# Performance work log

Measured on AMD Instinct MI355X. Metric: run time of the kernel, lower is better.

The kernel has to match this reference:

```python
import jax, jax.numpy as jnp
import numpy as np

N_HEAD = 16
HEAD_DIM = 64
ROPE_BASE = 10000.0


def _rope(t):
    # t: [B, H, C, D]; rotate-half RoPE, offset 0
    B, H, C, D = t.shape
    inv_freq = 1.0 / (ROPE_BASE ** (jnp.arange(0, D, 2, dtype=jnp.float32) / D))  # [D/2]
    ang = jnp.arange(C, dtype=jnp.float32)[:, None] * inv_freq[None, :]           # [C, D/2]
    cos = jnp.concatenate([jnp.cos(ang), jnp.cos(ang)], axis=-1)                  # [C, D]
    sin = jnp.concatenate([jnp.sin(ang), jnp.sin(ang)], axis=-1)                  # [C, D]
    t1, t2 = jnp.split(t, 2, axis=-1)
    rot = jnp.concatenate([-t2, t1], axis=-1)
    return t * cos.astype(t.dtype) + rot * sin.astype(t.dtype)


def setup_inputs() -> dict:
    key = jax.random.key(0)
    ks = jax.random.split(key, 5)
    E = 1024
    B, C = 2, 2048
    s = 1.0 / np.sqrt(E)
    return {
        "x": jax.random.normal(ks[0], (B, C, E), dtype=jnp.float32),
        "Wq": jax.random.normal(ks[1], (E, E), dtype=jnp.float32) * s,
        "Wk": jax.random.normal(ks[2], (E, E), dtype=jnp.float32) * s,
        "Wv": jax.random.normal(ks[3], (E, E), dtype=jnp.float32) * s,
        "Wo": jax.random.normal(ks[4], (E, E), dtype=jnp.float32) * s,
    }


def reference(x, Wq, Wk, Wv, Wo):
    B, C, E = x.shape
    H, D = N_HEAD, HEAD_DIM
    # nn.Linear(bias=False): y = x @ W.T
    Q = (x @ Wq.T).reshape(B, C, H, D).transpose(0, 2, 1, 3)  # [B,H,C,D]
    K = (x @ Wk.T).reshape(B, C, H, D).transpose(0, 2, 1, 3)
    V = (x @ Wv.T).reshape(B, C, H, D).transpose(0, 2, 1, 3)
    Q = _rope(Q)
    K = _rope(K)
    scores = jnp.einsum("bhqd,bhkd->bhqk", Q, K) / jnp.sqrt(jnp.float32(D))
    causal = jnp.tril(jnp.ones((C, C), dtype=bool))
    scores = jnp.where(causal, scores, jnp.float32(-jnp.inf))
    weights = jax.nn.softmax(scores, axis=-1)
    hidden = jnp.einsum("bhqk,bhkd->bhqd", weights, V)
    hidden = hidden.transpose(0, 2, 1, 3).reshape(B, C, H * D)
    return hidden @ Wo.T
```

## Files before the change

kernel.cpp:

```cpp
#include <hip/hip_runtime.h>
#include <hip/hip_bf16.h>

typedef __attribute__((ext_vector_type(8))) short bf16x8;
typedef __attribute__((ext_vector_type(4))) float f32x4;
typedef unsigned short u16;
typedef unsigned int u32;


__device__ __forceinline__ u16 f2bf(float f) {
  __hip_bfloat16 h = __float2bfloat16(f);
  return *reinterpret_cast<u16*>(&h);
}

__device__ __forceinline__ void async16(const void* g, void* l) {
  __builtin_amdgcn_global_load_lds((const __attribute__((address_space(1))) u32*)g,
                                   (__attribute__((address_space(3))) u32*)l, 16, 0, 0);
}


__global__ void cast_bf16(const float4* __restrict__ src, ushort4* __restrict__ dst, int n4) {
  int stride = gridDim.x * blockDim.x;
  for (int i = blockIdx.x * blockDim.x + threadIdx.x; i < n4; i += stride) {
    float4 v = src[i];
    ushort4 o;
    o.x = f2bf(v.x); o.y = f2bf(v.y); o.z = f2bf(v.z); o.w = f2bf(v.w);
    dst[i] = o;
  }
}

__global__ void cast_w4(const float4* __restrict__ w0, const float4* __restrict__ w1,
                        const float4* __restrict__ w2, const float4* __restrict__ w3,
                        ushort4* __restrict__ o0, ushort4* __restrict__ o1,
                        ushort4* __restrict__ o2, ushort4* __restrict__ o3, int n4) {
  const float4* src = (blockIdx.y == 0) ? w0 : (blockIdx.y == 1) ? w1 : (blockIdx.y == 2) ? w2 : w3;
  ushort4* dst = (blockIdx.y == 0) ? o0 : (blockIdx.y == 1) ? o1 : (blockIdx.y == 2) ? o2 : o3;
  int stride = gridDim.x * blockDim.x;
  for (int i = blockIdx.x * blockDim.x + threadIdx.x; i < n4; i += stride) {
    float4 v = src[i];
    ushort4 o;
    o.x = f2bf(v.x); o.y = f2bf(v.y); o.z = f2bf(v.z); o.w = f2bf(v.w);
    dst[i] = o;
  }
}


__global__ void rope_table(float* __restrict__ tcos, float* __restrict__ tsin) {
  int idx = blockIdx.x * blockDim.x + threadIdx.x;
  if (idx >= 2048 * 32) return;
  int c = idx >> 5, j = idx & 31;
  float inv = powf(10000.f, -(float)j * (1.f / 32.f));
  float ang = (float)c * inv;
  tcos[idx] = cosf(ang);
  tsin[idx] = sinf(ang);
}


__launch_bounds__(256)
__global__ void qkv_gemm(const u16* __restrict__ xb, const u16* __restrict__ Wqb,
                         const u16* __restrict__ Wkb, const u16* __restrict__ Wvb,
                         const float* __restrict__ tcos, const float* __restrict__ tsin,
                         u16* __restrict__ Qr, u16* __restrict__ Kr, u16* __restrict__ Vt) {
  const int z = blockIdx.z;
  const u16* W = (z == 0) ? Wqb : (z == 1) ? Wkb : Wvb;
  u16* dst = (z == 0) ? Qr : (z == 1) ? Kr : Vt;
  const int m0 = blockIdx.y * 128, n0 = blockIdx.x * 128;
  const int tid = threadIdx.x, w = tid >> 6, lane = tid & 63, g = lane >> 4, cl = lane & 15;
  const int wr = w >> 1, wc = w & 1;
  __shared__ u16 As[128][32], Bs[128][32];
  f32x4 acc[4][4] = {};
  for (int k0 = 0; k0 < 1024; k0 += 32) {
#pragma unroll
    for (int ch = 0; ch < 2; ++ch) {
      int t = tid + ch * 256;
      int row = t >> 2, col = (t & 3) * 8;
      async16(&xb[(size_t)(m0 + row) * 1024 + k0 + col], &As[row][col]);
      async16(&W[(size_t)(n0 + row) * 1024 + k0 + col], &Bs[row][col]);
    }
    __syncthreads();
    bf16x8 af[4], bfr[4];
#pragma unroll
    for (int i = 0; i < 4; ++i) af[i] = *(const bf16x8*)&As[wr * 64 + i * 16 + cl][g * 8];
#pragma unroll
    for (int j = 0; j < 4; ++j) bfr[j] = *(const bf16x8*)&Bs[wc * 64 + j * 16 + cl][g * 8];
#pragma unroll
    for (int i = 0; i < 4; ++i)
#pragma unroll
      for (int j = 0; j < 4; ++j)
        acc[i][j] = __builtin_amdgcn_mfma_f32_16x16x32_bf16(af[i], bfr[j], acc[i][j], 0, 0, 0);
    __syncthreads();
  }
  if (z < 2) {
#pragma unroll
    for (int i = 0; i < 4; ++i) {
      int mbase = m0 + wr * 64 + i * 16 + g * 4;
#pragma unroll
      for (int r = 0; r < 4; ++r) {
        int mm = mbase + r;
        int b = mm >> 11, pos = mm & 2047;
#pragma unroll
        for (int j = 0; j < 2; ++j) {
          int n = n0 + wc * 64 + j * 16 + cl;
          int h = n >> 6, dlo = n & 63;
          float a = acc[i][j][r], b2 = acc[i][j + 2][r];
          float cv = tcos[pos * 32 + dlo], sv = tsin[pos * 32 + dlo];
          float o1 = a * cv - b2 * sv;
          float o2 = b2 * cv + a * sv;
          size_t base = ((size_t)(b * 16 + h) * 2048 + pos) * 64;
          dst[base + dlo] = f2bf(o1);
          dst[base + dlo + 32] = f2bf(o2);
        }
      }
    }
  } else {
#pragma unroll
    for (int i = 0; i < 4; ++i) {
      int mbase = m0 + wr * 64 + i * 16 + g * 4;
      int b = mbase >> 11, pos = mbase & 2047;
#pragma unroll
      for (int j = 0; j < 4; ++j) {
        int n = n0 + wc * 64 + j * 16 + cl;
        int h = n >> 6, d = n & 63;
        ushort4 v4;
        v4.x = f2bf(acc[i][j][0]);
        v4.y = f2bf(acc[i][j][1]);
        v4.z = f2bf(acc[i][j][2]);
        v4.w = f2bf(acc[i][j][3]);
        *(ushort4*)&dst[((size_t)(b * 16 + h) * 64 + d) * 2048 + pos] = v4;
      }
    }
  }
}


__launch_bounds__(128)
__global__ void attn_kernel(const u16* __restrict__ Qr, const u16* __restrict__ Kr,
                            const u16* __restrict__ Vt, u16* __restrict__ hid) {
  const int bid = blockIdx.x;
  const int xcd = bid & 7, jj = bid >> 3;
  const int bh = xcd * 4 + (jj >> 5);
  const int p = jj & 31;
  const int wid = threadIdx.x >> 6;
  const int qt = wid ? p : 63 - p;
  const int lane = threadIdx.x & 63, g = lane >> 4, cl = lane & 15;
  const int b = bh >> 4, h = bh & 15;
  const int qbase = qt * 32;
  const u16* Qp = Qr + (size_t)bh * 2048 * 64;
  const u16* Kp = Kr + (size_t)bh * 2048 * 64;
  const u16* Vp = Vt + (size_t)bh * 2048 * 64;
  __shared__ u16 P_all[2][32 * 64];
  u16* P_lds = P_all[wid];

  bf16x8 aq[4];
#pragma unroll
  for (int qg = 0; qg < 2; ++qg)
#pragma unroll
    for (int ks = 0; ks < 2; ++ks)
      aq[qg * 2 + ks] = *(const bf16x8*)&Qp[(size_t)(qbase + qg * 16 + cl) * 64 + ks * 32 + g * 8];

  f32x4 ot[8] = {};
  float mrow[8], lrow[8];
#pragma unroll
  for (int r = 0; r < 8; ++r) { mrow[r] = -__builtin_inff(); lrow[r] = 0.f; }

  const int ktmax = qt >> 1;

  auto loadK = [&](bf16x8* dst, int kt_) {
#pragma unroll
    for (int n = 0; n < 4; ++n)
#pragma unroll
      for (int ks = 0; ks < 2; ++ks)
        dst[n * 2 + ks] = *(const bf16x8*)&Kp[(size_t)(kt_ * 64 + n * 16 + cl) * 64 + ks * 32 + g * 8];
  };
  auto loadV = [&](bf16x8* dst, int kt_) {
#pragma unroll
    for (int ks = 0; ks < 2; ++ks)
#pragma unroll
      for (int j = 0; j < 4; ++j)
        dst[ks * 4 + j] = *(const bf16x8*)&Vp[(size_t)(j * 16 + cl) * 2048 + kt_ * 64 + ks * 32 + g * 8];
  };

  auto tile = [&](const bf16x8* kf, const bf16x8* bv, int kt_, bool diag) {
    f32x4 s[8] = {};
#pragma unroll
    for (int qg = 0; qg < 2; ++qg)
#pragma unroll
      for (int n = 0; n < 4; ++n)
#pragma unroll
        for (int ks = 0; ks < 2; ++ks)
          s[qg * 4 + n] = __builtin_amdgcn_mfma_f32_16x16x32_bf16(aq[qg * 2 + ks], kf[n * 2 + ks],
                                                                  s[qg * 4 + n], 0, 0, 0);
    if (diag) {
#pragma unroll
      for (int qg = 0; qg < 2; ++qg)
#pragma unroll
        for (int n = 0; n < 4; ++n)
#pragma unroll
          for (int r = 0; r < 4; ++r) {
            int q = qbase + qg * 16 + g * 4 + r, k = kt_ * 64 + n * 16 + cl;
            s[qg * 4 + n][r] = (k <= q) ? s[qg * 4 + n][r] * 0.125f : -__builtin_inff();
          }
    } else {
#pragma unroll
      for (int i = 0; i < 8; ++i)
#pragma unroll
        for (int r = 0; r < 4; ++r) s[i][r] *= 0.125f;
    }
    bf16x8 ap[4];
#pragma unroll
    for (int qg = 0; qg < 2; ++qg) {
      float pmax[4], ef[4];
#pragma unroll
      for (int r = 0; r < 4; ++r) {
        float v = fmaxf(fmaxf(s[qg * 4 + 0][r], s[qg * 4 + 1][r]),
                        fmaxf(s[qg * 4 + 2][r], s[qg * 4 + 3][r]));
#pragma unroll
        for (int off = 1; off < 16; off <<= 1) v = fmaxf(v, __shfl_xor(v, off));
        pmax[r] = v;
      }
#pragma unroll
      for (int r = 0; r < 4; ++r) {
        float mnew = fmaxf(mrow[qg * 4 + r], pmax[r]);
        ef[r] = __expf(mrow[qg * 4 + r] - mnew);
        mrow[qg * 4 + r] = mnew;
      }
      float rs[4] = {0.f, 0.f, 0.f, 0.f};
#pragma unroll
      for (int n = 0; n < 4; ++n)
#pragma unroll
        for (int r = 0; r < 4; ++r) {
          float p2 = __expf(s[qg * 4 + n][r] - mrow[qg * 4 + r]);
          s[qg * 4 + n][r] = p2;
          rs[r] += p2;
          int row = qg * 16 + g * 4 + r;
          P_lds[(row * 64 + n * 16 + cl) ^ ((row & 7) << 3)] = f2bf(p2);
        }
#pragma unroll
      for (int r = 0; r < 4; ++r) {
        float v = rs[r];
#pragma unroll
        for (int off = 1; off < 16; off <<= 1) v += __shfl_xor(v, off);
        lrow[qg * 4 + r] = lrow[qg * 4 + r] * ef[r] + v;
      }
      int src = ((cl >> 2) << 4) | cl;
      float t0 = __shfl(ef[0], src), t1 = __shfl(ef[1], src);
      float t2 = __shfl(ef[2], src), t3 = __shfl(ef[3], src);
      float eft = (cl & 2) ? ((cl & 1) ? t3 : t2) : ((cl & 1) ? t1 : t0);
#pragma unroll
      for (int j = 0; j < 4; ++j)
#pragma unroll
        for (int r = 0; r < 4; ++r) ot[qg * 4 + j][r] *= eft;
#pragma unroll
      for (int ks = 0; ks < 2; ++ks) {
        int rowr = qg * 16 + cl;
        ap[qg * 2 + ks] = *(const bf16x8*)&P_lds[(rowr * 64 + ks * 32 + g * 8) ^ ((rowr & 7) << 3)];
      }
    }
#pragma unroll
    for (int qg = 0; qg < 2; ++qg)
#pragma unroll
      for (int ks = 0; ks < 2; ++ks)
#pragma unroll
        for (int j = 0; j < 4; ++j)
          ot[qg * 4 + j] = __builtin_amdgcn_mfma_f32_16x16x32_bf16(bv[ks * 4 + j], ap[qg * 2 + ks],
                                                                   ot[qg * 4 + j], 0, 0, 0);
  };

  bf16x8 kA[8], kB[8], bv[8];
  loadK(kA, 0);
  for (int kt = 0; kt <= ktmax; kt += 2) {
    loadV(bv, kt);
    if (kt + 1 <= ktmax) loadK(kB, kt + 1);
    tile(kA, bv, kt, kt == ktmax);
    if (kt + 1 <= ktmax) {
      loadV(bv, kt + 1);
      if (kt + 2 <= ktmax) loadK(kA, kt + 2);
      tile(kB, bv, kt + 1, kt + 1 == ktmax);
    }
  }

#pragma unroll
  for (int qg = 0; qg < 2; ++qg) {
    int src = ((cl >> 2) << 4) | cl;
    float t0 = __shfl(lrow[qg * 4 + 0], src), t1 = __shfl(lrow[qg * 4 + 1], src);
    float t2 = __shfl(lrow[qg * 4 + 2], src), t3 = __shfl(lrow[qg * 4 + 3], src);
    float lt = (cl & 2) ? ((cl & 1) ? t3 : t2) : ((cl & 1) ? t1 : t0);
    float inv = 1.f / lt;
    int q = qbase + qg * 16 + cl;
#pragma unroll
    for (int j = 0; j < 4; ++j) {
      ushort4 v4;
      v4.x = f2bf(ot[qg * 4 + j][0] * inv);
      v4.y = f2bf(ot[qg * 4 + j][1] * inv);
      v4.z = f2bf(ot[qg * 4 + j][2] * inv);
      v4.w = f2bf(ot[qg * 4 + j][3] * inv);
      *(ushort4*)&hid[((size_t)(b * 2048) + q) * 1024 + h * 64 + j * 16 + g * 4] = v4;
    }
  }
}


__launch_bounds__(256)
__global__ void out_gemm(const u16* __restrict__ hb, const u16* __restrict__ Wob,
                         float* __restrict__ out) {
  const int m0 = blockIdx.y * 128, n0 = blockIdx.x * 128;
  const int tid = threadIdx.x, w = tid >> 6, lane = tid & 63, g = lane >> 4, cl = lane & 15;
  const int wr = w >> 1, wc = w & 1;
  __shared__ u16 As[128][32], Bs[128][32];
  f32x4 acc[4][4] = {};
  for (int k0 = 0; k0 < 1024; k0 += 32) {
#pragma unroll
    for (int ch = 0; ch < 2; ++ch) {
      int t = tid + ch * 256;
      int row = t >> 2, col = (t & 3) * 8;
      async16(&hb[(size_t)(m0 + row) * 1024 + k0 + col], &As[row][col]);
      async16(&Wob[(size_t)(n0 + row) * 1024 + k0 + col], &Bs[row][col]);
    }
    __syncthreads();
    bf16x8 af[4], bfr[4];
#pragma unroll
    for (int i = 0; i < 4; ++i) af[i] = *(const bf16x8*)&As[wr * 64 + i * 16 + cl][g * 8];
#pragma unroll
    for (int j = 0; j < 4; ++j) bfr[j] = *(const bf16x8*)&Bs[wc * 64 + j * 16 + cl][g * 8];
#pragma unroll
    for (int i = 0; i < 4; ++i)
#pragma unroll
      for (int j = 0; j < 4; ++j)
        acc[i][j] = __builtin_amdgcn_mfma_f32_16x16x32_bf16(af[i], bfr[j], acc[i][j], 0, 0, 0);
    __syncthreads();
  }
#pragma unroll
  for (int i = 0; i < 4; ++i)
#pragma unroll
    for (int r = 0; r < 4; ++r) {
      int m = m0 + wr * 64 + i * 16 + g * 4 + r;
#pragma unroll
      for (int j = 0; j < 4; ++j)
        out[(size_t)m * 1024 + n0 + wc * 64 + j * 16 + cl] = acc[i][j][r];
    }
}


extern "C" void kernel_launch(void* const* d_in, const int* in_sizes, int n_in,
                              void* d_out, int out_size, void* d_ws, size_t ws_size,
                              hipStream_t stream) {
  const float* x = (const float*)d_in[0];
  const float* Wq = (const float*)d_in[1];
  const float* Wk = (const float*)d_in[2];
  const float* Wv = (const float*)d_in[3];
  const float* Wo = (const float*)d_in[4];
  float* out = (float*)d_out;

  char* ws = (char*)d_ws;
  size_t off = 0;
  auto alloc = [&](size_t bytes) {
    void* p = ws + off;
    off += (bytes + 255) & ~(size_t)255;
    return p;
  };
  u16* xb = (u16*)alloc(4096ull * 1024 * 2);
  u16* Wqb = (u16*)alloc(1024ull * 1024 * 2);
  u16* Wkb = (u16*)alloc(1024ull * 1024 * 2);
  u16* Wvb = (u16*)alloc(1024ull * 1024 * 2);
  u16* Wob = (u16*)alloc(1024ull * 1024 * 2);
  u16* Qr = (u16*)alloc(4096ull * 1024 * 2);
  u16* Kr = (u16*)alloc(4096ull * 1024 * 2);
  u16* Vt = (u16*)alloc(4096ull * 1024 * 2);
  u16* hid = (u16*)alloc(4096ull * 1024 * 2);
  float* tcos = (float*)alloc(2048ull * 32 * 4);
  float* tsin = (float*)alloc(2048ull * 32 * 4);

  cast_bf16<<<1024, 256, 0, stream>>>((const float4*)x, (ushort4*)xb, 4096 * 1024 / 4);
  cast_w4<<<dim3(256, 4), 256, 0, stream>>>((const float4*)Wq, (const float4*)Wk,
                                            (const float4*)Wv, (const float4*)Wo,
                                            (ushort4*)Wqb, (ushort4*)Wkb,
                                            (ushort4*)Wvb, (ushort4*)Wob, 1024 * 1024 / 4);
  rope_table<<<256, 256, 0, stream>>>(tcos, tsin);

  qkv_gemm<<<dim3(8, 32, 3), 256, 0, stream>>>(xb, Wqb, Wkb, Wvb, tcos, tsin, Qr, Kr, Vt);
  attn_kernel<<<1024, 128, 0, stream>>>(Qr, Kr, Vt, hid);
  out_gemm<<<dim3(8, 32), 256, 0, stream>>>(hid, Wob, out);
}
```

Before: 276.4 us.

## Split key range across two waves per query tile with LDS merge; use exp2 softmax

Each block now handles one 32-row query tile, and its two waves take alternating key tiles (split-K) instead of each wave owning a separate query tile paired for causal balance. Wave 1 writes its partial output, max and sum to shared memory, and wave 0 merges them with log-sum-exp rescaling before storing. The grid is doubled to 2048 blocks. The softmax scale is folded with log2(e) so exp2f replaces __expf. The split adds a sync, LDS traffic and a merge step, and short tiles leave one wave idle.

Result: no change. 272.5 us (-1.4%).

```diff
diff --git a/kernel.cpp b/kernel.cpp
--- a/kernel.cpp
+++ b/kernel.cpp
@@ -5,6 +5,8 @@
 typedef __attribute__((ext_vector_type(4))) float f32x4;
 typedef unsigned short u16;
 typedef unsigned int u32;
+
+#define SM_SCALE 0.18033688f
 
 
 __device__ __forceinline__ u16 f2bf(float f) {
@@ -137,10 +139,9 @@
                             const u16* __restrict__ Vt, u16* __restrict__ hid) {
   const int bid = blockIdx.x;
   const int xcd = bid & 7, jj = bid >> 3;
-  const int bh = xcd * 4 + (jj >> 5);
-  const int p = jj & 31;
+  const int bh = xcd * 4 + (jj >> 6);
+  const int qt = 63 - (jj & 63);
   const int wid = threadIdx.x >> 6;
-  const int qt = wid ? p : 63 - p;
   const int lane = threadIdx.x & 63, g = lane >> 4, cl = lane & 15;
   const int b = bh >> 4, h = bh & 15;
   const int qbase = qt * 32;
@@ -148,6 +149,8 @@
   const u16* Kp = Kr + (size_t)bh * 2048 * 64;
   const u16* Vp = Vt + (size_t)bh * 2048 * 64;
   __shared__ u16 P_all[2][32 * 64];
+  __shared__ float Osh[64][33];
+  __shared__ float Msh[32][2];
   u16* P_lds = P_all[wid];
 
   bf16x8 aq[4];
@@ -197,13 +200,13 @@
 #pragma unroll
           for (int r = 0; r < 4; ++r) {
             int q = qbase + qg * 16 + g * 4 + r, k = kt_ * 64 + n * 16 + cl;
-            s[qg * 4 + n][r] = (k <= q) ? s[qg * 4 + n][r] * 0.125f : -__builtin_inff();
+            s[qg * 4 + n][r] = (k <= q) ? s[qg * 4 + n][r] * SM_SCALE : -__builtin_inff();
           }
     } else {
 #pragma unroll
       for (int i = 0; i < 8; ++i)
 #pragma unroll
-        for (int r = 0; r < 4; ++r) s[i][r] *= 0.125f;
+        for (int r = 0; r < 4; ++r) s[i][r] *= SM_SCALE;
     }
     bf16x8 ap[4];
 #pragma unroll
@@ -220,7 +223,7 @@
 #pragma unroll
       for (int r = 0; r < 4; ++r) {
         float mnew = fmaxf(mrow[qg * 4 + r], pmax[r]);
-        ef[r] = __expf(mrow[qg * 4 + r] - mnew);
+        ef[r] = exp2f(mrow[qg * 4 + r] - mnew);
         mrow[qg * 4 + r] = mnew;
       }
       float rs[4] = {0.f, 0.f, 0.f, 0.f};
@@ -228,7 +231,7 @@
       for (int n = 0; n < 4; ++n)
 #pragma unroll
         for (int r = 0; r < 4; ++r) {
-          float p2 = __expf(s[qg * 4 + n][r] - mrow[qg * 4 + r]);
+          float p2 = exp2f(s[qg * 4 + n][r] - mrow[qg * 4 + r]);
           s[qg * 4 + n][r] = p2;
           rs[r] += p2;
           int row = qg * 16 + g * 4 + r;
@@ -266,34 +269,66 @@
   };
 
   bf16x8 kA[8], kB[8], bv[8];
-  loadK(kA, 0);
-  for (int kt = 0; kt <= ktmax; kt += 2) {
-    loadV(bv, kt);
-    if (kt + 1 <= ktmax) loadK(kB, kt + 1);
-    tile(kA, bv, kt, kt == ktmax);
-    if (kt + 1 <= ktmax) {
-      loadV(bv, kt + 1);
-      if (kt + 2 <= ktmax) loadK(kA, kt + 2);
-      tile(kB, bv, kt + 1, kt + 1 == ktmax);
-    }
-  }
-
-#pragma unroll
-  for (int qg = 0; qg < 2; ++qg) {
-    int src = ((cl >> 2) << 4) | cl;
-    float t0 = __shfl(lrow[qg * 4 + 0], src), t1 = __shfl(lrow[qg * 4 + 1], src);
-    float t2 = __shfl(lrow[qg * 4 + 2], src), t3 = __shfl(lrow[qg * 4 + 3], src);
-    float lt = (cl & 2) ? ((cl & 1) ? t3 : t2) : ((cl & 1) ? t1 : t0);
-    float inv = 1.f / lt;
-    int q = qbase + qg * 16 + cl;
-#pragma unroll
-    for (int j = 0; j < 4; ++j) {
-      ushort4 v4;
-      v4.x = f2bf(ot[qg * 4 + j][0] * inv);
-      v4.y = f2bf(ot[qg * 4 + j][1] * inv);
-      v4.z = f2bf(ot[qg * 4 + j][2] * inv);
-      v4.w = f2bf(ot[qg * 4 + j][3] * inv);
-      *(ushort4*)&hid[((size_t)(b * 2048) + q) * 1024 + h * 64 + j * 16 + g * 4] = v4;
+  const int kts = wid;
+  if (kts <= ktmax) {
+    loadK(kA, kts);
+    for (int kt = kts; kt <= ktmax; kt += 4) {
+      loadV(bv, kt);
+      if (kt + 2 <= ktmax) loadK(kB, kt + 2);
+      tile(kA, bv, kt, kt == ktmax);
+      if (kt + 2 <= ktmax) {
+        loadV(bv, kt + 2);
+        if (kt + 4 <= ktmax) loadK(kA, kt + 4);
+        tile(kB, bv, kt + 2, kt + 2 == ktmax);
+      }
+    }
+  }
+
+  if (wid == 1) {
+#pragma unroll
+    for (int qg = 0; qg < 2; ++qg)
+#pragma unroll
+      for (int j = 0; j < 4; ++j)
+#pragma unroll
+        for (int r = 0; r < 4; ++r)
+          Osh[j * 16 + g * 4 + r][qg * 16 + cl] = ot[qg * 4 + j][r];
+    if (cl == 0) {
+#pragma unroll
+      for (int qg = 0; qg < 2; ++qg)
+#pragma unroll
+        for (int r = 0; r < 4; ++r) {
+          Msh[qg * 16 + g * 4 + r][0] = mrow[qg * 4 + r];
+          Msh[qg * 16 + g * 4 + r][1] = lrow[qg * 4 + r];
+        }
+    }
+  }
+  __syncthreads();
+  if (wid == 0) {
+#pragma unroll
+    for (int qg = 0; qg < 2; ++qg) {
+      int src = ((cl >> 2) << 4) | cl;
+      float m0 = __shfl(mrow[qg * 4 + 0], src), m1_ = __shfl(mrow[qg * 4 + 1], src);
+      float m2 = __shfl(mrow[qg * 4 + 2], src), m3 = __shfl(mrow[qg * 4 + 3], src);
+      float m0t = (cl & 2) ? ((cl & 1) ? m3 : m2) : ((cl & 1) ? m1_ : m0);
+      float l0 = __shfl(lrow[qg * 4 + 0], src), l1_ = __shfl(lrow[qg * 4 + 1], src);
+      float l2 = __shfl(lrow[qg * 4 + 2], src), l3 = __shfl(lrow[qg * 4 + 3], src);
+      float l0t = (cl & 2) ? ((cl & 1) ? l3 : l2) : ((cl & 1) ? l1_ : l0);
+      int q = qg * 16 + cl;
+      float m1t = Msh[q][0], l1t = Msh[q][1];
+      float mm = fmaxf(m0t, m1t);
+      float a0 = exp2f(m0t - mm), a1 = exp2f(m1t - mm);
+      float linv = 1.f / (l0t * a0 + l1t * a1);
+      float s0 = a0 * linv, s1 = a1 * linv;
+      int qglob = qbase + q;
+#pragma unroll
+      for (int j = 0; j < 4; ++j) {
+        ushort4 v4;
+        v4.x = f2bf(ot[qg * 4 + j][0] * s0 + Osh[j * 16 + g * 4 + 0][q] * s1);
+        v4.y = f2bf(ot[qg * 4 + j][1] * s0 + Osh[j * 16 + g * 4 + 1][q] * s1);
+        v4.z = f2bf(ot[qg * 4 + j][2] * s0 + Osh[j * 16 + g * 4 + 2][q] * s1);
+        v4.w = f2bf(ot[qg * 4 + j][3] * s0 + Osh[j * 16 + g * 4 + 3][q] * s1);
+        *(ushort4*)&hid[((size_t)(b * 2048) + qglob) * 1024 + h * 64 + j * 16 + g * 4] = v4;
+      }
     }
   }
 }
@@ -377,6 +412,6 @@
   rope_table<<<256, 256, 0, stream>>>(tcos, tsin);
 
   qkv_gemm<<<dim3(8, 32, 3), 256, 0, stream>>>(xb, Wqb, Wkb, Wvb, tcos, tsin, Qr, Kr, Vt);
-  attn_kernel<<<1024, 128, 0, stream>>>(Qr, Kr, Vt, hid);
+  attn_kernel<<<2048, 128, 0, stream>>>(Qr, Kr, Vt, hid);
   out_gemm<<<dim3(8, 32), 256, 0, stream>>>(hid, Wob, out);
 }
```
